# Kernel tuning notes

Measured on AMD Instinct MI355X. Metric: run time of the kernel, lower is better.

Reference implementation:

```python
import jax, jax.numpy as jnp
import numpy as np

S = 64        # state_size (nodes per graph == feature width)
B = 1024      # number of graphs
N = B * S     # total nodes
DEG = 16      # avg degree
E = N * DEG   # total edges
A = 16        # attractors
EPS = 1e-5


def setup_inputs() -> dict:
    key = jax.random.key(0)
    ks = jax.random.split(key, 16)
    x = jax.random.normal(ks[0], (N, 1), dtype=jnp.float32)
    # block-diagonal batched graphs: each graph has S nodes, S*DEG edges
    epg = S * DEG
    gid = jnp.arange(E, dtype=jnp.int32) // epg
    src = gid * S + jax.random.randint(ks[1], (E,), 0, S, dtype=jnp.int32)
    dst = gid * S + jax.random.randint(ks[2], (E,), 0, S, dtype=jnp.int32)
    edge_index = jnp.stack([src, dst], axis=0)
    f32 = jnp.float32
    return {
        "x": x, "edge_index": edge_index,
        # EdgeConv MLP: Linear(2,4) -> ReLU -> Linear(4,S)
        "w1": jax.random.normal(ks[3], (2, 4), f32) * 0.5,
        "b1": jnp.zeros((4,), f32),
        "w2": jax.random.normal(ks[4], (4, S), f32) * 0.3,
        "b2": jnp.zeros((S,), f32),
        # Conv1d(S,S,3,padding=1) x2
        "conv2_w": jax.random.normal(ks[5], (S, S, 3), f32) / np.sqrt(3 * S),
        "conv2_b": jnp.zeros((S,), f32),
        "conv3_w": jax.random.normal(ks[6], (S, S, 3), f32) / np.sqrt(3 * S),
        "conv3_b": jnp.zeros((S,), f32),
        # BatchNorm affine params
        "g1": jnp.ones((S,), f32), "be1": jnp.zeros((S,), f32),
        "g2": jnp.ones((S,), f32), "be2": jnp.zeros((S,), f32),
        "g3": jnp.ones((S,), f32), "be3": jnp.zeros((S,), f32),
        # MLP tail
        "wm1": jax.random.normal(ks[7], (S * S, 256), f32) / np.sqrt(S * S),
        "bm1": jnp.zeros((256,), f32),
        "wm2": jax.random.normal(ks[8], (256, 256), f32) / 16.0,
        "bm2": jnp.zeros((256,), f32),
        "wm3": jax.random.normal(ks[9], (256, 256), f32) / 16.0,
        "bm3": jnp.zeros((256,), f32),
        "wp": jax.random.normal(ks[10], (256, A), f32) / 16.0,
        "bp": jnp.zeros((A,), f32),
    }


def _bn(h, gamma, beta, axes):
    # training-mode batch norm (biased variance), per-channel
    mean = jnp.mean(h, axis=axes, keepdims=True)
    var = jnp.mean(jnp.square(h - mean), axis=axes, keepdims=True)
    inv = jax.lax.rsqrt(var + EPS)
    sh = [1] * h.ndim
    sh[1] = -1
    return (h - mean) * inv * gamma.reshape(sh) + beta.reshape(sh)


def _conv1d(h, w, b):
    # h: [B, C, L], w: [O, I, K], padding=1 -> same length
    out = jax.lax.conv_general_dilated(
        h, w, window_strides=(1,), padding=((1, 1),),
        dimension_numbers=("NCH", "OIH", "NCH"))
    return out + b[None, :, None]


def reference(x, edge_index, w1, b1, w2, b2, conv2_w, conv2_b, conv3_w, conv3_b,
              g1, be1, g2, be2, g3, be3, wm1, bm1, wm2, bm2, wm3, bm3, wp, bp):
    src, dst = edge_index[0], edge_index[1]
    # EdgeConv (aggr='add'): nn(cat[x_i, x_j - x_i]) summed at target i
    xi = x[dst]                              # [E,1] gather
    xj = x[src]                              # [E,1] gather
    m = jnp.concatenate([xi, xj - xi], axis=-1)      # [E,2]
    m = jax.nn.relu(m @ w1 + b1)                     # [E,4]
    m = m @ w2 + b2                                   # [E,S]
    out = jax.ops.segment_sum(m, dst, num_segments=N)  # [N,S] scatter-add
    # BN1 + ReLU on [N,S] (channel dim = 1)
    out = jax.nn.relu(_bn(out, g1, be1, axes=(0,)))
    # per-graph feature map: [B, S_nodes, S_feat] -> channels-first [B,S,S]
    out = out.reshape(B, S, S).swapaxes(1, 2)
    out = jax.nn.relu(_bn(_conv1d(out, conv2_w, conv2_b), g2, be2, axes=(0, 2)))
    out = jax.nn.relu(_bn(_conv1d(out, conv3_w, conv3_b), g3, be3, axes=(0, 2)))
    out = out.reshape(B, S * S)
    out = jax.nn.relu(out @ wm1 + bm1)
    out = jax.nn.relu(out @ wm2 + bm2)
    out = jax.nn.relu(out @ wm3 + bm3)
    logits = out @ wp + bp                            # [B, A]
    return jax.nn.log_softmax(logits, axis=1)
```

## Files before the change

kernel.cpp:

```cpp
#include <hip/hip_runtime.h>
#include <cstdint>
#include <cstddef>

typedef __attribute__((ext_vector_type(8))) short short8;
typedef __attribute__((ext_vector_type(8))) unsigned short ushort8;
typedef __attribute__((ext_vector_type(4))) float f32x4;

#define EPSV 1e-5f
#define NB 1024
#define NEDGE 1048576
#define EPG 1024
#define CNTF 65536.0f
#define REP 32


__device__ __forceinline__ ushort f2bf(float f) {
  uint u = __float_as_uint(f);
  return (ushort)((u + 0x7FFFu + ((u >> 16) & 1u)) >> 16);
}
__device__ __forceinline__ float bf2f(ushort u) {
  return __uint_as_float((uint)u << 16);
}

__global__ __launch_bounds__(256) void k_prepw(
    const float* __restrict__ wm1, const float* __restrict__ wm2,
    const float* __restrict__ wm3, const float* __restrict__ wp,
    const float* __restrict__ c2w, const float* __restrict__ c3w,
    ushort* __restrict__ wbf1t, ushort* __restrict__ wbf2t,
    ushort* __restrict__ wbf3t, ushort* __restrict__ wptbf,
    ushort* __restrict__ cwt2, ushort* __restrict__ cwt3,
    float* __restrict__ stats)
{
  __shared__ ushort T[64][72];
  const int tid = threadIdx.x;
  const int bb = blockIdx.x;

  if (bb < 256) {
    const int kc = bb >> 2, n0 = (bb & 3) << 6;
    const int kk = tid >> 2, np = (tid & 3) << 4;
    const float* srow = wm1 + (((size_t)(kk << 6) + kc) << 8) + n0 + np;
#pragma unroll
    for (int i = 0; i < 4; ++i) {
      const float4 v = *(const float4*)(srow + (i << 2));
      const int n = np + (i << 2);
      T[n + 0][kk] = f2bf(v.x); T[n + 1][kk] = f2bf(v.y);
      T[n + 2][kk] = f2bf(v.z); T[n + 3][kk] = f2bf(v.w);
    }
    __syncthreads();
    ushort* dst = wbf1t + ((size_t)kc << 14) + (n0 << 6);
    const int nl = tid >> 2, qk = (tid & 3) << 4;
    *(ushort8*)(dst + (nl << 6) + qk) = *(ushort8*)&T[nl][qk];
    *(ushort8*)(dst + (nl << 6) + qk + 8) = *(ushort8*)&T[nl][qk + 8];
    return;
  }
  if (bb < 320) {
    const int base = (((bb - 256) << 8) + tid) << 3;
    const int m = base >> 16;
    const int rem = base & 65535;
    const int kc = rem >> 14, within = rem & 16383;
    const int n = within >> 6, kk0 = within & 63;
    const float* src = m ? wm3 : wm2;
    ushort* dst = m ? wbf3t : wbf2t;
    ushort tmp[8];
#pragma unroll
    for (int j = 0; j < 8; ++j)
      tmp[j] = f2bf(src[(((kc << 6) | (kk0 + j)) << 8) + n]);
    *(ushort8*)&dst[rem] = *(ushort8*)&tmp[0];
    return;
  }
  if (bb == 320) {
    const int a = tid & 15, k0 = (tid >> 4) << 4;
    ushort tmp[16];
#pragma unroll
    for (int j = 0; j < 16; ++j) tmp[j] = f2bf(wp[((k0 + j) << 4) + a]);
    *(ushort8*)&wptbf[(a << 8) + k0] = *(ushort8*)&tmp[0];
    *(ushort8*)&wptbf[(a << 8) + k0 + 8] = *(ushort8*)&tmp[8];
    return;
  }
  if (bb == 417) {
    float4 z4 = make_float4(0.f, 0.f, 0.f, 0.f);
#pragma unroll
    for (int i = 0; i < 12; ++i) ((float4*)stats)[(i << 8) + tid] = z4;
    return;
  }
  const int flat = (bb - 321) * 256 + tid;
  const int m = flat >= 12288;
  const int idx = flat - (m ? 12288 : 0);
  const float* src = m ? c3w : c2w;
  ushort* dst = m ? cwt3 : cwt2;
  const int o = idx / 192, rem = idx - o * 192;
  const int kk = rem >> 6, c = rem & 63;
  dst[idx] = f2bf(src[o * 192 + c * 3 + kk]);
}

__global__ __launch_bounds__(256) void k_edge(
    const float* __restrict__ x, const int* __restrict__ ei,
    const float* __restrict__ w1, const float* __restrict__ b1,
    const float* __restrict__ w2, const float* __restrict__ b2,
    ushort* __restrict__ out0, float* __restrict__ stats1)
{
  __shared__ float xs[64];
  __shared__ float aggT[4][5][72];
  __shared__ float aggC[64][8];
  __shared__ float w1s[8], b1s[4];
  __shared__ float w2s[256], b2s[64];
  __shared__ float rs[4][64], rss[4][64];
  const int tid = threadIdx.x;
  const int b = blockIdx.x;
  const int w = tid >> 6;

  if (tid < 8) w1s[tid] = w1[tid];
  if (tid < 4) b1s[tid] = b1[tid];
  if (tid < 64) { xs[tid] = x[(b << 6) + tid]; b2s[tid] = b2[tid]; }
  w2s[tid] = w2[tid];
  for (int i = tid; i < 1440; i += 256) ((float*)aggT)[i] = 0.f;
  __syncthreads();

  const int e0 = b * EPG;
  const int4 s4 = ((const int4*)(ei + e0))[tid];
  const int4 d4 = ((const int4*)(ei + NEDGE + e0))[tid];
  float* agw = &aggT[w][0][0];
  const int sls[4] = {s4.x & 63, s4.y & 63, s4.z & 63, s4.w & 63};
  const int dls[4] = {d4.x & 63, d4.y & 63, d4.z & 63, d4.w & 63};
#pragma unroll
  for (int e = 0; e < 4; ++e) {
    const int dl = dls[e];
    const float xi = xs[dl];
    const float dx = xs[sls[e]] - xi;
#pragma unroll
    for (int j = 0; j < 4; ++j) {
      float h = fmaxf(fmaf(xi, w1s[j], fmaf(dx, w1s[4 + j], b1s[j])), 0.f);
      atomicAdd(&agw[j * 72 + dl], h);
    }
    atomicAdd(&agw[4 * 72 + dl], 1.0f);
  }
  __syncthreads();

  if (tid < 64) {
    const int n = tid;
    const float a0 = aggT[0][0][n] + aggT[1][0][n] + aggT[2][0][n] + aggT[3][0][n];
    const float a1 = aggT[0][1][n] + aggT[1][1][n] + aggT[2][1][n] + aggT[3][1][n];
    const float a2 = aggT[0][2][n] + aggT[1][2][n] + aggT[2][2][n] + aggT[3][2][n];
    const float a3v = aggT[0][3][n] + aggT[1][3][n] + aggT[2][3][n] + aggT[3][3][n];
    const float dg = aggT[0][4][n] + aggT[1][4][n] + aggT[2][4][n] + aggT[3][4][n];
    *(float4*)&aggC[n][0] = make_float4(a0, a1, a2, a3v);
    aggC[n][4] = dg;
  }
  __syncthreads();

  const int c = tid & 63, qq = tid >> 6;
  const float wc0 = w2s[c], wc1 = w2s[64 + c], wc2 = w2s[128 + c], wc3 = w2s[192 + c];
  const float b2c = b2s[c];
  float s = 0.f, ss = 0.f;
  for (int n = qq; n < 64; n += 4) {
    const float4 a = *(const float4*)&aggC[n][0];
    const float dg = aggC[n][4];
    float v = a.x * wc0 + a.y * wc1 + a.z * wc2 + a.w * wc3 + dg * b2c;
    out0[(size_t)(((b << 6) + n) << 6) + c] = f2bf(v);
    s += v; ss += v * v;
  }
  rs[qq][c] = s; rss[qq][c] = ss;
  __syncthreads();
  if (tid < 64) {
    float* dst = stats1 + ((b & (REP - 1)) << 7);
    atomicAdd(&dst[tid], rs[0][tid] + rs[1][tid] + rs[2][tid] + rs[3][tid]);
    atomicAdd(&dst[64 + tid], rss[0][tid] + rss[1][tid] + rss[2][tid] + rss[3][tid]);
  }
}

__global__ __launch_bounds__(256) void k_convm(
    const ushort* __restrict__ in,
    const float* __restrict__ stats_in,
    const float* __restrict__ gamma, const float* __restrict__ beta,
    const ushort* __restrict__ cwt, const float* __restrict__ cb,
    ushort* __restrict__ out,
    float* __restrict__ stats_out)
{
  __shared__ ushort As[64][200];
  __shared__ ushort Yt[66][72];
  __shared__ float aco[64], bco[64], cbs[64];
  __shared__ float ldsS[64], ldsSS[64];
  const int tid = threadIdx.x;
  const int b = blockIdx.x;

  if (tid < 64) {
    float sm = 0.f, sq = 0.f;
#pragma unroll 8
    for (int r = 0; r < REP; ++r) {
      sm += stats_in[(r << 7) + tid];
      sq += stats_in[(r << 7) + 64 + tid];
    }
    const float mean = sm * (1.0f / CNTF);
    const float var = sq * (1.0f / CNTF) - mean * mean;
    const float a = gamma[tid] * rsqrtf(var + EPSV);
    aco[tid] = a;
    bco[tid] = beta[tid] - mean * a;
    cbs[tid] = cb[tid];
    Yt[0][tid] = 0;
    Yt[65][tid] = 0;
  }
  __syncthreads();

  const size_t base = (size_t)b << 12;
  {
    const int lr = tid >> 2, p = (tid & 3) << 4;
    const ushort8 r0 = *(const ushort8*)&in[base + (lr << 6) + p];
    const ushort8 r1 = *(const ushort8*)&in[base + (lr << 6) + p + 8];
    ushort tmp[16];
#pragma unroll
    for (int j = 0; j < 8; ++j)
      tmp[j] = f2bf(fmaxf(fmaf(aco[p + j], bf2f(r0[j]), bco[p + j]), 0.f));
#pragma unroll
    for (int j = 0; j < 8; ++j)
      tmp[8 + j] = f2bf(fmaxf(fmaf(aco[p + 8 + j], bf2f(r1[j]), bco[p + 8 + j]), 0.f));
    *(ushort8*)&Yt[lr + 1][p] = *(ushort8*)&tmp[0];
    *(ushort8*)&Yt[lr + 1][p + 8] = *(ushort8*)&tmp[8];
  }
  {
    const ushort8* gw = (const ushort8*)cwt;
#pragma unroll
    for (int i = 0; i < 6; ++i) {
      const int e8 = (i << 8) + tid;
      const int o = e8 / 24, k8 = (e8 - o * 24) << 3;
      *(ushort8*)&As[o][k8] = gw[e8];
    }
  }
  __syncthreads();

  const int lane = tid & 63, w = tid >> 6;
  const int lm = lane & 15, q = lane >> 4;
  f32x4 acc[4];
#pragma unroll
  for (int nt = 0; nt < 4; ++nt) acc[nt] = (f32x4){0.f, 0.f, 0.f, 0.f};

#pragma unroll
  for (int kk = 0; kk < 3; ++kk) {
#pragma unroll
    for (int ks = 0; ks < 2; ++ks) {
      const short8 af = *(const short8*)&As[(w << 4) + lm][(kk << 6) + (ks << 5) + (q << 3)];
#pragma unroll
      for (int nt = 0; nt < 4; ++nt) {
        const short8 bfr = *(const short8*)&Yt[(nt << 4) + lm + kk][(ks << 5) + (q << 3)];
        acc[nt] = __builtin_amdgcn_mfma_f32_16x16x32_bf16(af, bfr, acc[nt], 0, 0, 0);
      }
    }
  }

  const int obase = (w << 4) + (q << 2);
  const float4 cb4 = *(const float4*)&cbs[obase];
  float s[4] = {0.f, 0.f, 0.f, 0.f}, ss[4] = {0.f, 0.f, 0.f, 0.f};
#pragma unroll
  for (int nt = 0; nt < 4; ++nt) {
    const int l = (nt << 4) + lm;
    float4 v = make_float4(acc[nt][0] + cb4.x, acc[nt][1] + cb4.y,
                           acc[nt][2] + cb4.z, acc[nt][3] + cb4.w);
    *(ushort4*)&out[base + (l << 6) + obase] =
        make_ushort4(f2bf(v.x), f2bf(v.y), f2bf(v.z), f2bf(v.w));
    s[0] += v.x; ss[0] += v.x * v.x;
    s[1] += v.y; ss[1] += v.y * v.y;
    s[2] += v.z; ss[2] += v.z * v.z;
    s[3] += v.w; ss[3] += v.w * v.w;
  }
#pragma unroll
  for (int i = 0; i < 4; ++i) {
#pragma unroll
    for (int off = 1; off < 16; off <<= 1) {
      s[i] += __shfl_xor(s[i], off);
      ss[i] += __shfl_xor(ss[i], off);
    }
    if (lm == 0) { ldsS[obase + i] = s[i]; ldsSS[obase + i] = ss[i]; }
  }
  __syncthreads();
  if (tid < 64) {
    float* dst = stats_out + ((b & (REP - 1)) << 7);
    atomicAdd(&dst[tid], ldsS[tid]);
    atomicAdd(&dst[64 + tid], ldsSS[tid]);
  }
}

__global__ __launch_bounds__(256) void k_mlp1(
    const ushort* __restrict__ z3, const float* __restrict__ stats3,
    const float* __restrict__ g3, const float* __restrict__ be3,
    const ushort* __restrict__ wbf1t, float* __restrict__ h1part)
{
  __shared__ ushort Ys[64][72];
  __shared__ ushort Ws[128][72];
  __shared__ float a3s[64], b3s[64];
  const int tid = threadIdx.x;
  const int bx = blockIdx.x, by = blockIdx.y, bz = blockIdx.z;

  if (tid < 64) {
    float sm = 0.f, sq = 0.f;
#pragma unroll 8
    for (int r = 0; r < REP; ++r) {
      sm += stats3[(r << 7) + tid];
      sq += stats3[(r << 7) + 64 + tid];
    }
    const float mean = sm * (1.0f / CNTF);
    const float var = sq * (1.0f / CNTF) - mean * mean;
    const float a = g3[tid] * rsqrtf(var + EPSV);
    a3s[tid] = a;
    b3s[tid] = be3[tid] - mean * a;
  }
  __syncthreads();

  const int lane = tid & 63, w = tid >> 6;
  const int lm = lane & 15, q = lane >> 4;
  const int gy = tid >> 2, py = (tid & 3) << 4;
  const int nn = tid >> 1, pp = (tid & 1) << 2;
  const int g0 = bx << 6, n0 = by << 7;

  f32x4 acc[8];
#pragma unroll
  for (int nt = 0; nt < 8; ++nt) acc[nt] = (f32x4){0.f, 0.f, 0.f, 0.f};

  const size_t ybase = ((size_t)(g0 + gy) << 12);

#pragma unroll 1
  for (int ck = 0; ck < 8; ++ck) {
    const int kc = (bz << 9) + (ck << 6);
    if (ck) __syncthreads();
    {
      const ushort* src = z3 + ybase + kc + py;
      const ushort8 r0 = *(const ushort8*)src;
      const ushort8 r1 = *(const ushort8*)(src + 8);
      ushort tmp[16];
#pragma unroll
      for (int j = 0; j < 8; ++j)
        tmp[j] = f2bf(fmaxf(fmaf(a3s[py + j], bf2f(r0[j]), b3s[py + j]), 0.f));
#pragma unroll
      for (int j = 0; j < 8; ++j)
        tmp[8 + j] = f2bf(fmaxf(fmaf(a3s[py + 8 + j], bf2f(r1[j]), b3s[py + 8 + j]), 0.f));
      *(ushort8*)&Ys[gy][py] = *(ushort8*)&tmp[0];
      *(ushort8*)&Ys[gy][py + 8] = *(ushort8*)&tmp[8];
    }
    {
      const ushort8* gw = (const ushort8*)(wbf1t + ((size_t)((bz << 3) + ck) << 14) + (n0 << 6));
#pragma unroll
      for (int i = 0; i < 4; ++i)
        *(ushort8*)&Ws[nn][(pp + i) << 3] = gw[(nn << 3) + pp + i];
    }
    __syncthreads();
#pragma unroll
    for (int ks = 0; ks < 2; ++ks) {
      const short8 af = *(const short8*)&Ys[(w << 4) + lm][(ks << 5) + (q << 3)];
#pragma unroll
      for (int nt = 0; nt < 8; ++nt) {
        const short8 bfr = *(const short8*)&Ws[(nt << 4) + lm][(ks << 5) + (q << 3)];
        acc[nt] = __builtin_amdgcn_mfma_f32_16x16x32_bf16(af, bfr, acc[nt], 0, 0, 0);
      }
    }
  }

  float* dst0 = h1part + ((size_t)bz << 18);
  const int gout = g0 + (w << 4) + (q << 2);
#pragma unroll
  for (int nt = 0; nt < 8; ++nt) {
    const int col = n0 + (nt << 4) + lm;
#pragma unroll
    for (int i = 0; i < 4; ++i)
      dst0[((size_t)(gout + i) << 8) + col] = acc[nt][i];
  }
}

__global__ __launch_bounds__(256) void k_tail(
    const float* __restrict__ h1part, const float* __restrict__ bm1,
    const ushort* __restrict__ wbf2t, const float* __restrict__ bm2,
    const ushort* __restrict__ wbf3t, const float* __restrict__ bm3,
    const ushort* __restrict__ wptbf, const float* __restrict__ bp,
    float* __restrict__ out)
{
  __shared__ ushort Ws[256][72];
  __shared__ ushort h1s[16][264];
  __shared__ ushort h2s[16][264];
  ushort* wpt = &Ws[0][0];
  const int tid = threadIdx.x;
  const int g0 = blockIdx.x << 4;
  const int lane = tid & 63, w = tid >> 6;
  const int lm = lane & 15, q = lane >> 4;
  const int gr = q << 2;

  {
    const int r = tid >> 4, c0 = (tid & 15) << 4;
    const float* srcb = h1part + ((size_t)(g0 + r) << 8) + c0;
#pragma unroll
    for (int i = 0; i < 4; ++i) {
      float4 vs = *(const float4*)(bm1 + c0 + (i << 2));
#pragma unroll
      for (int bz = 0; bz < 8; ++bz) {
        const float4 p = *(const float4*)(srcb + ((size_t)bz << 18) + (i << 2));
        vs.x += p.x; vs.y += p.y; vs.z += p.z; vs.w += p.w;
      }
      *(ushort4*)&h1s[r][c0 + (i << 2)] = make_ushort4(
          f2bf(fmaxf(vs.x, 0.f)), f2bf(fmaxf(vs.y, 0.f)),
          f2bf(fmaxf(vs.z, 0.f)), f2bf(fmaxf(vs.w, 0.f)));
    }
  }

  f32x4 acc[4];
#pragma unroll
  for (int nt = 0; nt < 4; ++nt) acc[nt] = (f32x4){0.f, 0.f, 0.f, 0.f};
#pragma unroll 1
  for (int ck = 0; ck < 4; ++ck) {
    __syncthreads();
    {
      const ushort8* gw = (const ushort8*)(wbf2t + (ck << 14));
#pragma unroll
      for (int i = 0; i < 8; ++i) {
        const int e8 = (i << 8) + tid;
        const int n = e8 >> 3, kk = (e8 & 7) << 3;
        *(ushort8*)&Ws[n][kk] = gw[e8];
      }
    }
    __syncthreads();
#pragma unroll
    for (int ks = 0; ks < 2; ++ks) {
      const short8 af = *(const short8*)&h1s[lm][(ck << 6) + (ks << 5) + (q << 3)];
#pragma unroll
      for (int nt = 0; nt < 4; ++nt) {
        const short8 bfr = *(const short8*)&Ws[(w << 6) + (nt << 4) + lm][(ks << 5) + (q << 3)];
        acc[nt] = __builtin_amdgcn_mfma_f32_16x16x32_bf16(af, bfr, acc[nt], 0, 0, 0);
      }
    }
  }
#pragma unroll
  for (int nt = 0; nt < 4; ++nt) {
    const int col = (w << 6) + (nt << 4) + lm;
    const float bv = bm2[col];
#pragma unroll
    for (int i = 0; i < 4; ++i)
      h2s[gr + i][col] = f2bf(fmaxf(acc[nt][i] + bv, 0.f));
  }

  f32x4 acc2[4];
#pragma unroll
  for (int nt = 0; nt < 4; ++nt) acc2[nt] = (f32x4){0.f, 0.f, 0.f, 0.f};
#pragma unroll 1
  for (int ck = 0; ck < 4; ++ck) {
    __syncthreads();
    {
      const ushort8* gw = (const ushort8*)(wbf3t + (ck << 14));
#pragma unroll
      for (int i = 0; i < 8; ++i) {
        const int e8 = (i << 8) + tid;
        const int n = e8 >> 3, kk = (e8 & 7) << 3;
        *(ushort8*)&Ws[n][kk] = gw[e8];
      }
    }
    __syncthreads();
#pragma unroll
    for (int ks = 0; ks < 2; ++ks) {
      const short8 af = *(const short8*)&h2s[lm][(ck << 6) + (ks << 5) + (q << 3)];
#pragma unroll
      for (int nt = 0; nt < 4; ++nt) {
        const short8 bfr = *(const short8*)&Ws[(w << 6) + (nt << 4) + lm][(ks << 5) + (q << 3)];
        acc2[nt] = __builtin_amdgcn_mfma_f32_16x16x32_bf16(af, bfr, acc2[nt], 0, 0, 0);
      }
    }
  }

  __syncthreads();
  {
    const ushort8* gw = (const ushort8*)wptbf;
#pragma unroll
    for (int i = 0; i < 2; ++i) {
      const int e8 = (i << 8) + tid;
      const int flat = e8 << 3;
      const int a = flat >> 8, kk = flat & 255;
      *(ushort8*)&wpt[a * 264 + kk] = gw[e8];
    }
  }
#pragma unroll
  for (int nt = 0; nt < 4; ++nt) {
    const int col = (w << 6) + (nt << 4) + lm;
    const float bv = bm3[col];
#pragma unroll
    for (int i = 0; i < 4; ++i)
      h2s[gr + i][col] = f2bf(fmaxf(acc2[nt][i] + bv, 0.f));
  }
  __syncthreads();

  if (w == 0) {
    f32x4 lacc = (f32x4){0.f, 0.f, 0.f, 0.f};
#pragma unroll
    for (int ks = 0; ks < 8; ++ks) {
      const short8 af = *(const short8*)&h2s[lm][(ks << 5) + (q << 3)];
      const short8 bfr = *(const short8*)&wpt[lm * 264 + (ks << 5) + (q << 3)];
      lacc = __builtin_amdgcn_mfma_f32_16x16x32_bf16(af, bfr, lacc, 0, 0, 0);
    }
    const float bpv = bp[lm];
    float lg[4], mx[4], se[4];
#pragma unroll
    for (int i = 0; i < 4; ++i) {
      lg[i] = lacc[i] + bpv;
      float m = lg[i];
#pragma unroll
      for (int off = 1; off < 16; off <<= 1) m = fmaxf(m, __shfl_xor(m, off));
      mx[i] = m;
      float e = expf(lg[i] - m);
#pragma unroll
      for (int off = 1; off < 16; off <<= 1) e += __shfl_xor(e, off);
      se[i] = e;
    }
#pragma unroll
    for (int i = 0; i < 4; ++i)
      out[((g0 + gr + i) << 4) + lm] = (lg[i] - mx[i]) - logf(se[i]);
  }
}

extern "C" void kernel_launch(void* const* d_in, const int* in_sizes, int n_in,
                              void* d_out, int out_size, void* d_ws, size_t ws_size,
                              hipStream_t stream)
{
  const float* x   = (const float*)d_in[0];
  const int*   ei  = (const int*)d_in[1];
  const float* w1  = (const float*)d_in[2];
  const float* b1  = (const float*)d_in[3];
  const float* w2  = (const float*)d_in[4];
  const float* b2  = (const float*)d_in[5];
  const float* c2w = (const float*)d_in[6];
  const float* c2b = (const float*)d_in[7];
  const float* c3w = (const float*)d_in[8];
  const float* c3b = (const float*)d_in[9];
  const float* g1  = (const float*)d_in[10];
  const float* be1 = (const float*)d_in[11];
  const float* g2  = (const float*)d_in[12];
  const float* be2 = (const float*)d_in[13];
  const float* g3  = (const float*)d_in[14];
  const float* be3 = (const float*)d_in[15];
  const float* wm1 = (const float*)d_in[16];
  const float* bm1 = (const float*)d_in[17];
  const float* wm2 = (const float*)d_in[18];
  const float* bm2 = (const float*)d_in[19];
  const float* wm3 = (const float*)d_in[20];
  const float* bm3 = (const float*)d_in[21];
  const float* wp  = (const float*)d_in[22];
  const float* bp  = (const float*)d_in[23];

  char* ws = (char*)d_ws;
  ushort* ubuf0 = (ushort*)ws;
  ushort* ubuf1 = (ushort*)(ws + ((size_t)8 << 20));
  float*  h1part = (float*)(ws + ((size_t)16 << 20));
  ushort* wbf1t = (ushort*)(ws + ((size_t)24 << 20));
  ushort* wbf2t = (ushort*)(ws + ((size_t)26 << 20));
  ushort* wbf3t = (ushort*)(ws + ((size_t)26 << 20) + (128 << 10));
  ushort* wptbf = (ushort*)(ws + ((size_t)26 << 20) + (256 << 10));
  float* stats = (float*)(ws + ((size_t)27 << 20));
  float* stats1 = stats;
  float* stats2 = stats + REP * 128;
  float* stats3 = stats + 2 * REP * 128;
  ushort* cwt2 = (ushort*)d_out;
  ushort* cwt3 = (ushort*)d_out + 12288;

  k_prepw<<<dim3(418), dim3(256), 0, stream>>>(
      wm1, wm2, wm3, wp, c2w, c3w,
      wbf1t, wbf2t, wbf3t, wptbf, cwt2, cwt3, stats);
  k_edge<<<dim3(NB), dim3(256), 0, stream>>>(x, ei, w1, b1, w2, b2, ubuf0, stats1);
  k_convm<<<dim3(NB), dim3(256), 0, stream>>>(ubuf0, stats1, g1, be1, cwt2, c2b, ubuf1, stats2);
  k_convm<<<dim3(NB), dim3(256), 0, stream>>>(ubuf1, stats2, g2, be2, cwt3, c3b, ubuf0, stats3);
  k_mlp1<<<dim3(16, 2, 8), dim3(256), 0, stream>>>(ubuf0, stats3, g3, be3, wbf1t, h1part);
  k_tail<<<dim3(64), dim3(256), 0, stream>>>(h1part, bm1, wbf2t, bm2, wbf3t, bm3,
                                             wptbf, bp, (float*)d_out);
}
```

Baseline: 186.0 us.

## Replace per-edge float atomics with integer edge-count matrix and dense aggregation

Each edge now does a single integer atomic increment into a 64x64 per-graph count matrix indexed by (dst, src), instead of five float atomics per edge into per-wave buffers. The hidden-layer sums are then rebuilt densely: each thread takes one (node, hidden unit) pair and loops over all 64 source nodes, weighting each ReLU hidden value by its edge count. This cuts LDS atomic traffic and contention and drops the cross-wave reduction step. In exchange it adds a 64x64 dense loop per thread, a larger shared-memory footprint, and more zeroing work.

```diff
diff --git a/kernel.cpp b/kernel.cpp
--- a/kernel.cpp
+++ b/kernel.cpp
@@ -100,51 +100,46 @@
     ushort* __restrict__ out0, float* __restrict__ stats1)
 {
   __shared__ float xs[64];
-  __shared__ float aggT[4][5][72];
+  __shared__ int   Mc[64][65];
   __shared__ float aggC[64][8];
   __shared__ float w1s[8], b1s[4];
   __shared__ float w2s[256], b2s[64];
   __shared__ float rs[4][64], rss[4][64];
   const int tid = threadIdx.x;
   const int b = blockIdx.x;
-  const int w = tid >> 6;
 
   if (tid < 8) w1s[tid] = w1[tid];
   if (tid < 4) b1s[tid] = b1[tid];
   if (tid < 64) { xs[tid] = x[(b << 6) + tid]; b2s[tid] = b2[tid]; }
   w2s[tid] = w2[tid];
-  for (int i = tid; i < 1440; i += 256) ((float*)aggT)[i] = 0.f;
+  for (int i = tid; i < 64 * 65; i += 256) ((int*)Mc)[i] = 0;
   __syncthreads();
 
   const int e0 = b * EPG;
   const int4 s4 = ((const int4*)(ei + e0))[tid];
   const int4 d4 = ((const int4*)(ei + NEDGE + e0))[tid];
-  float* agw = &aggT[w][0][0];
-  const int sls[4] = {s4.x & 63, s4.y & 63, s4.z & 63, s4.w & 63};
-  const int dls[4] = {d4.x & 63, d4.y & 63, d4.z & 63, d4.w & 63};
-#pragma unroll
-  for (int e = 0; e < 4; ++e) {
-    const int dl = dls[e];
-    const float xi = xs[dl];
-    const float dx = xs[sls[e]] - xi;
-#pragma unroll
-    for (int j = 0; j < 4; ++j) {
-      float h = fmaxf(fmaf(xi, w1s[j], fmaf(dx, w1s[4 + j], b1s[j])), 0.f);
-      atomicAdd(&agw[j * 72 + dl], h);
-    }
-    atomicAdd(&agw[4 * 72 + dl], 1.0f);
-  }
-  __syncthreads();
-
-  if (tid < 64) {
-    const int n = tid;
-    const float a0 = aggT[0][0][n] + aggT[1][0][n] + aggT[2][0][n] + aggT[3][0][n];
-    const float a1 = aggT[0][1][n] + aggT[1][1][n] + aggT[2][1][n] + aggT[3][1][n];
-    const float a2 = aggT[0][2][n] + aggT[1][2][n] + aggT[2][2][n] + aggT[3][2][n];
-    const float a3v = aggT[0][3][n] + aggT[1][3][n] + aggT[2][3][n] + aggT[3][3][n];
-    const float dg = aggT[0][4][n] + aggT[1][4][n] + aggT[2][4][n] + aggT[3][4][n];
-    *(float4*)&aggC[n][0] = make_float4(a0, a1, a2, a3v);
-    aggC[n][4] = dg;
+  atomicAdd(&Mc[d4.x & 63][s4.x & 63], 1);
+  atomicAdd(&Mc[d4.y & 63][s4.y & 63], 1);
+  atomicAdd(&Mc[d4.z & 63][s4.z & 63], 1);
+  atomicAdd(&Mc[d4.w & 63][s4.w & 63], 1);
+  __syncthreads();
+
+  {
+    const int n = tid & 63, j = tid >> 6;
+    const float xn = xs[n];
+    const float bj = w1s[4 + j];
+    const float alpha = fmaf(xn, w1s[j] - bj, b1s[j]);
+    float acc = 0.f;
+    int dg = 0;
+#pragma unroll 8
+    for (int m = 0; m < 64; ++m) {
+      const int c = Mc[n][m];
+      const float h = fmaxf(fmaf(bj, xs[m], alpha), 0.f);
+      acc += (float)c * h;
+      dg += c;
+    }
+    aggC[n][j] = acc;
+    if (j == 0) aggC[n][4] = (float)dg;
   }
   __syncthreads();
 
```

Result: faster. 166.3 us (-10.6%).
